# Performance work log

Measured on AMD Instinct MI355X. Metric: run time of the kernel, lower is better.

Reference implementation:

```python
import jax, jax.numpy as jnp
import numpy as np
from jax.scipy.special import gammaln

T_STEPS, N_GRID, NMUL = 730, 10000, 2
NEARZERO = 1e-5
LENF = 15  # unit-hydrograph length used by UH_gamma routing
STAT_NAMES = ["parFC", "parK0", "parK1", "parK2", "parLP", "parPERC", "parUZL",
              "parTT", "parCFMAX", "parCFR", "parCWH", "parC", "parRT", "parAC"]
BOUNDS = {"parBETA": (1.0, 6.0), "parFC": (50.0, 1000.0), "parK0": (0.05, 0.9),
          "parK1": (0.01, 0.5), "parK2": (0.001, 0.2), "parLP": (0.2, 1.0),
          "parPERC": (0.0, 10.0), "parUZL": (0.0, 100.0), "parTT": (-2.5, 2.5),
          "parCFMAX": (0.5, 10.0), "parCFR": (0.0, 0.1), "parCWH": (0.0, 0.2),
          "parBETAET": (0.3, 5.0), "parC": (0.0, 1.0), "parRT": (0.0, 20.0),
          "parAC": (0.0, 2500.0)}
ROUT_A = (0.0, 2.9)
ROUT_B = (0.0, 6.5)


def _scale(p, lo, hi):
    # change_param_range: affine map of [0,1]-normalized params to physical bounds
    return p * (hi - lo) + lo


def setup_inputs() -> dict:
    key = jax.random.key(0)
    ks = jax.random.split(key, 7)
    prcp = jax.random.uniform(ks[0], (T_STEPS, N_GRID)) * 10.0          # mm/day
    tmean = jax.random.uniform(ks[1], (T_STEPS, N_GRID)) * 30.0 - 10.0  # deg C, spans parTT range
    pet = jax.random.uniform(ks[2], (T_STEPS, N_GRID)) * 5.0            # mm/day
    x_phy = jnp.stack([prcp, tmean, pet], axis=-1).astype(jnp.float32)
    ac_all = jax.random.uniform(ks[3], (N_GRID,)) * 2500.0              # drainage area per unit basin
    elev_all = jax.random.uniform(ks[4], (N_GRID,)) * 3000.0            # elevation
    params_dy = jax.random.uniform(ks[5], (T_STEPS, N_GRID, 2 * NMUL))  # dynamic: parBETA, parBETAET
    params_stat = jax.random.uniform(ks[6], (N_GRID, 14 * NMUL + 2))    # 14 static phy + 2 routing
    return {"x_phy": x_phy, "ac_all": ac_all, "elev_all": elev_all,
            "params_dy": params_dy, "params_stat": params_stat}


def _forward(x_phy, ac_all, elev_all, params_dy, params_stat):
    T, G, _ = x_phy.shape
    P, Tair, PET = x_phy[..., 0], x_phy[..., 1], x_phy[..., 2]
    # expand forcing to nmul parameter components
    Pm = jnp.broadcast_to(P[..., None], (T, G, NMUL))
    Tm = jnp.broadcast_to(Tair[..., None], (T, G, NMUL))
    PETm = jnp.broadcast_to(PET[..., None], (T, G, NMUL))
    Ac = jnp.broadcast_to(ac_all[:, None], (G, NMUL))

    # dynamic (per-timestep) params; dy_drop=0.0 -> bernoulli drop mask is all zeros,
    # so the dynamic values are used directly at every step
    dy = params_dy.reshape(T, G, 2, NMUL)
    parBETA = _scale(dy[:, :, 0], *BOUNDS["parBETA"])
    parBETAET = _scale(dy[:, :, 1], *BOUNDS["parBETAET"])

    # static params: [G, 14, NMUL]
    stat = params_stat[:, :14 * NMUL].reshape(G, 14, NMUL)
    sp = {n: _scale(stat[:, i], *BOUNDS[n]) for i, n in enumerate(STAT_NAMES)}
    rout_a = _scale(params_stat[:, 14 * NMUL], *ROUT_A)
    rout_b = _scale(params_stat[:, 14 * NMUL + 1], *ROUT_B)

    def step(carry, xt):
        SNOWPACK, MELTWATER, SM, SUZ, SLZ = carry
        Pt, Tt, PETt, beta, betaet = xt
        rain_mask = (Tt >= sp["parTT"]).astype(Pt.dtype)
        RAIN = Pt * rain_mask
        SNOW = Pt * (1.0 - rain_mask)
        # --- snow bucket ---
        SNOWPACK = SNOWPACK + SNOW
        melt = jnp.maximum(sp["parCFMAX"] * (Tt - sp["parTT"]), 0.0)
        melt = jnp.minimum(melt, SNOWPACK)
        MELTWATER = MELTWATER + melt
        SNOWPACK = SNOWPACK - melt
        refreeze = jnp.maximum(sp["parCFR"] * sp["parCFMAX"] * (sp["parTT"] - Tt), 0.0)
        refreeze = jnp.minimum(refreeze, MELTWATER)
        SNOWPACK = SNOWPACK + refreeze
        MELTWATER = MELTWATER - refreeze
        tosoil = jnp.maximum(MELTWATER - sp["parCWH"] * SNOWPACK, 0.0)
        MELTWATER = MELTWATER - tosoil
        # --- soil bucket ---
        soil_wetness = jnp.clip((SM / sp["parFC"]) ** beta, 0.0, 1.0)
        recharge = (RAIN + tosoil) * soil_wetness
        SM = SM + RAIN + tosoil - recharge
        excess = jnp.maximum(SM - sp["parFC"], 0.0)
        SM = SM - excess
        evapfactor = jnp.clip(SM / (sp["parLP"] * sp["parFC"]), 0.0, 1.0) ** betaet
        ETact = jnp.minimum(SM, PETt * evapfactor)
        SM = jnp.maximum(SM - ETact, NEARZERO)
        # capillary rise from lower groundwater zone (parC)
        capillary = jnp.minimum(SLZ, sp["parC"] * SLZ * (1.0 - jnp.minimum(SM / sp["parFC"], 1.0)))
        SM = jnp.maximum(SM + capillary, NEARZERO)
        SLZ = jnp.maximum(SLZ - capillary, NEARZERO)
        # --- groundwater buckets ---
        SUZ = SUZ + recharge + excess
        PERC = jnp.minimum(SUZ, sp["parPERC"])
        SUZ = SUZ - PERC
        Q0 = sp["parK0"] * jnp.maximum(SUZ - sp["parUZL"], 0.0)
        SUZ = SUZ - Q0
        Q1 = sp["parK1"] * SUZ
        SUZ = SUZ - Q1
        SLZ = SLZ + PERC
        # HBV 2.0 regional groundwater loss (area-dependent via parRT / parAC; reconstructed)
        gw_loss = jnp.minimum(SLZ, sp["parRT"] * jnp.clip(1.0 - Ac / (sp["parAC"] + NEARZERO), 0.0, 1.0))
        SLZ = SLZ - gw_loss
        Q2 = sp["parK2"] * SLZ
        SLZ = SLZ - Q2
        Qt = Q0 + Q1 + Q2
        return (SNOWPACK, MELTWATER, SM, SUZ, SLZ), Qt

    init = tuple(jnp.full((G, NMUL), 1e-3, dtype=x_phy.dtype) for _ in range(5))
    _, Qsimmu = jax.lax.scan(step, init, (Pm, Tm, PETm, parBETA, parBETAET))
    Qsim = Qsimmu.mean(-1)  # [T, G]; muwts=None -> uniform average over nmul components

    # --- gamma unit-hydrograph routing (UH_gamma + causal UH_conv) ---
    a = jnp.maximum(rout_a, 0.0) + 0.1       # [G]
    theta = jnp.maximum(rout_b, 0.0) + 0.5   # [G]
    t = jnp.arange(LENF, dtype=Qsim.dtype) + 0.5  # [LENF]
    w = (jnp.exp(-gammaln(a))[None, :] * theta[None, :] ** (-a[None, :])
         * t[:, None] ** (a[None, :] - 1.0) * jnp.exp(-t[:, None] / theta[None, :]))
    w = w / w.sum(0)  # [LENF, G], normalized UH weights
    # causal grouped conv: flow[t] = sum_k w[k] * Qsim[t-k]
    Qpad = jnp.pad(Qsim, ((LENF - 1, 0), (0, 0)))
    flow = jnp.zeros_like(Qsim)
    for k in range(LENF):  # fixed, small tap count
        flow = flow + w[k][None, :] * Qpad[LENF - 1 - k: LENF - 1 - k + T]
    return flow[..., None]  # [T, G, 1] routed streamflow


def reference(x_phy, ac_all, elev_all, params_dy, params_stat):
    return _forward(x_phy, ac_all, elev_all, params_dy, params_stat)
```

## Files before the change

### kernel.cpp

```cpp
#include <hip/hip_runtime.h>


#define TS 730
#define NG 10000
#define CH 15
#define NCHUNK 49
#define XSTRIDE (NG * 3)
#define DSTRIDE (NG * 4)

#define AS1 __attribute__((address_space(1)))
#define AS3 __attribute__((address_space(3)))
#define WAIT_VMCNT(n) __builtin_amdgcn_s_waitcnt(((n) & 15) | 0x70 | 0xF00 | (((n) >> 4) << 14))
#define WAIT_LGKM0    __builtin_amdgcn_s_waitcnt(0xC07F)
#define SBAR          __builtin_amdgcn_s_barrier
#define SCHED_FENCE() __builtin_amdgcn_sched_barrier(0)

__device__ __forceinline__ void gload16(const float* g, float* l) {
    __builtin_amdgcn_global_load_lds((const AS1 void*)g, (AS3 void*)l, 16, 0, 0);
}
__device__ __forceinline__ float powpos(float x, float b) {
    return __builtin_amdgcn_exp2f(b * __builtin_amdgcn_logf(x));
}
__device__ __forceinline__ float med3(float x, float lo, float hi) {
    return __builtin_amdgcn_fmed3f(x, lo, hi);
}

__global__ __launch_bounds__(128, 1) void hbv_fused(
    const float* __restrict__ x_phy,
    const float* __restrict__ ac_all,
    const float* __restrict__ params_dy,
    const float* __restrict__ params_stat,
    float* __restrict__ out)
{
    __shared__ float xls0[1536], xls1[1536];
    __shared__ float dls0[2048], dls1[2048];
    __shared__ float qb0[960], qb1[960];

    const int tid  = threadIdx.x;
    const int wid  = tid >> 6;
    const int lane = tid & 63;
    const int m    = lane >> 5;
    const int cell = lane & 31;
    const int g0   = blockIdx.x * 32;
    const int g    = g0 + cell;
    const int gl   = g < NG ? g : NG - 1;
    const int g0r  = (g0 <= NG - 32) ? g0 : NG - 32;
    const int co   = cell + (g0 - g0r);
    const int cl   = co < 31 ? co : 31;

    const float* ps = params_stat + (size_t)gl * 30;
    const float FC    = ps[0  + m] * 950.f   + 50.f;
    const float K0    = ps[2  + m] * 0.85f   + 0.05f;
    const float K1    = ps[4  + m] * 0.49f   + 0.01f;
    const float K2    = ps[6  + m] * 0.199f  + 0.001f;
    const float LP    = ps[8  + m] * 0.8f    + 0.2f;
    const float PERCp = ps[10 + m] * 10.f;
    const float UZL   = ps[12 + m] * 100.f;
    const float TTp   = ps[14 + m] * 5.f     - 2.5f;
    const float CFMAX = ps[16 + m] * 9.5f    + 0.5f;
    const float CFR   = ps[18 + m] * 0.1f;
    const float CWH   = ps[20 + m] * 0.2f;
    const float Cc    = ps[22 + m];
    const float RT    = ps[24 + m] * 20.f;
    const float ACp   = ps[26 + m] * 2500.f;
    const float ra    = ps[28] * 2.9f;
    const float rb    = ps[29] * 6.5f;

    const float Acv     = ac_all[gl];
    const float invFC   = 1.f / FC;
    const float invLPFC = 1.f / (LP * FC);
    const float nCFRC   = -(CFR * CFMAX);
    const float gwcap   = RT * fminf(fmaxf(1.f - Acv / (ACp + 1e-5f), 0.f), 1.f);

    const float a     = fmaxf(ra, 0.f) + 0.1f;
    const float th    = fmaxf(rb, 0.f) + 0.5f;
    const float am1   = a - 1.f;
    const float nl2e  = 1.44269504f / th;
    float w[CH];
    float wsum = 0.f;
#pragma unroll
    for (int k = 0; k < CH; ++k) {
        const float tk = (float)k + 0.5f;
        const float v  = __builtin_amdgcn_exp2f(am1 * __builtin_amdgcn_logf(tk) - tk * nl2e);
        w[k] = v; wsum += v;
    }
    const float wn = 0.5f / wsum;
#pragma unroll
    for (int k = 0; k < CH; ++k) w[k] *= wn;

    int offx[6], offd[8];
#pragma unroll
    for (int i = 0; i < 6; ++i) {
        int idx = i * 64 + lane;
        idx = idx < 360 ? idx : 359;
        const int row = idx / 24;
        const int col = idx - row * 24;
        offx[i] = row * XSTRIDE + col * 4;
    }
#pragma unroll
    for (int i = 0; i < 8; ++i) {
        int idx = i * 64 + lane;
        idx = idx < 480 ? idx : 479;
        const int row = idx >> 5;
        const int col = idx & 31;
        offd[i] = row * DSTRIDE + col * 4;
    }
    const float* xbase = x_phy     + (size_t)g0r * 3;
    const float* dbase = params_dy + (size_t)g0r * 4;

    auto issue = [&](int cc, float* xl, float* dl) {
        if (cc == NCHUNK - 1) {
#pragma unroll
            for (int i = 0; i < 6; ++i) {
                int idx = i * 64 + lane; idx = idx < 360 ? idx : 359;
                const int row = idx / 24, col = idx - row * 24;
                int t = cc * CH + row; t = t < TS ? t : TS - 1;
                gload16(xbase + (size_t)t * XSTRIDE + col * 4, xl + i * 256);
            }
#pragma unroll
            for (int i = 0; i < 8; ++i) {
                int idx = i * 64 + lane; idx = idx < 480 ? idx : 479;
                const int row = idx >> 5, col = idx & 31;
                int t = cc * CH + row; t = t < TS ? t : TS - 1;
                gload16(dbase + (size_t)t * DSTRIDE + col * 4, dl + i * 256);
            }
        } else {
            const float* xp = xbase + (size_t)cc * CH * XSTRIDE;
            const float* dp = dbase + (size_t)cc * CH * DSTRIDE;
#pragma unroll
            for (int i = 0; i < 6; ++i) gload16(xp + offx[i], xl + i * 256);
#pragma unroll
            for (int i = 0; i < 8; ++i) gload16(dp + offd[i], dl + i * 256);
        }
    };

    if (wid == 0) {
        float SP = 1e-3f, MW = 1e-3f, SM = 1e-3f, SUZ = 1e-3f, SLZ = 1e-3f;
        float CcSLZ = Cc * 1e-3f;

        auto scan = [&](const float* xl, const float* dl, float* qb) {
            float Pc = xl[cl * 3 + 0], Tc = xl[cl * 3 + 1], Ec = xl[cl * 3 + 2];
            float4 dvc = *(const float4*)&dl[cl * 4];
#pragma unroll
            for (int j = 0; j < CH; ++j) {
                float Pn, Tn, En; float4 dvn;
                if (j < CH - 1) {
                    Pn  = xl[(j + 1) * 96 + cl * 3 + 0];
                    Tn  = xl[(j + 1) * 96 + cl * 3 + 1];
                    En  = xl[(j + 1) * 96 + cl * 3 + 2];
                    dvn = *(const float4*)&dl[(j + 1) * 128 + cl * 4];
                }
                const float beta   = fmaf(m ? dvc.y : dvc.x, 5.f, 1.f);
                const float betaet = fmaf(m ? dvc.w : dvc.z, 4.7f, 0.3f);

                const float t1   = Tc - TTp;
                const float snow = (t1 < 0.f) ? Pc : 0.f;
                const float rain = Pc - snow;
                SP += snow;
                const float melt = med3(CFMAX * t1, 0.f, SP);
                MW += melt; SP -= melt;
                const float refr = med3(nCFRC * t1, 0.f, MW);
                SP += refr; MW -= refr;
                const float tosoil = fmaxf(MW - CWH * SP, 0.f);
                MW -= tosoil;

                const float sw  = fminf(powpos(SM * invFC, beta), 1.f);
                const float rts = rain + tosoil;
                SM = fmaf(rts, 1.f - sw, SM);
                const float exc = fmaxf(SM - FC, 0.f);
                SM = fminf(SM, FC);
                const float ef = powpos(fminf(SM * invLPFC, 1.f), betaet);
                SM = fmaxf(SM - Ec * ef, 1e-5f);
                const float cap = CcSLZ * fmaxf(1.f - SM * invFC, 0.f);
                SM  = fmaxf(SM + cap, 1e-5f);
                SLZ = fmaxf(SLZ - cap, 1e-5f);

                SUZ = SUZ + rts * sw + exc;
                const float perc = fminf(SUZ, PERCp);
                SUZ -= perc;
                const float Q0 = K0 * fmaxf(SUZ - UZL, 0.f);
                SUZ -= Q0;
                const float Q1 = K1 * SUZ;
                SUZ -= Q1;
                SLZ += perc;
                SLZ = fmaxf(SLZ - gwcap, 0.f);
                const float Q2 = K2 * SLZ;
                SLZ -= Q2;
                CcSLZ = Cc * SLZ;
                qb[(j << 6) + lane] = Q0 + Q1 + Q2;

                Pc = Pn; Tc = Tn; Ec = En; dvc = dvn;
            }
        };

        SBAR();
        scan(xls0, dls0, qb0);
        WAIT_LGKM0; SCHED_FENCE();
        for (int cp = 0; cp < 24; ++cp) {
            SBAR();
            scan(xls1, dls1, qb1);
            WAIT_LGKM0; SCHED_FENCE();
            SBAR();
            scan(xls0, dls0, qb0);
            WAIT_LGKM0; SCHED_FENCE();
        }
        SBAR();
    } else {
        float facc[CH];
#pragma unroll
        for (int k = 0; k < CH; ++k) facc[k] = 0.f;
        const bool doStore = (g < NG) && (lane < 32);
        const int  l32 = lane & 31;

        auto conv = [&](int c, const float* qb) {
            float* op = out + (size_t)c * CH * NG + g;
            const int tb = c * CH;
#pragma unroll
            for (int j = 0; j < CH; ++j) {
                const float qm = qb[(j << 6) + l32] + qb[(j << 6) + 32 + l32];
#pragma unroll
                for (int k = 0; k < CH; ++k)
                    facc[(j + k) % CH] = fmaf(w[k], qm, facc[(j + k) % CH]);
                if (doStore && (tb + j < TS)) op[(size_t)j * NG] = facc[j];
                facc[j] = 0.f;
            }
        };

        issue(0, xls0, dls0);
        WAIT_VMCNT(0); SCHED_FENCE();
        SBAR();
        issue(1, xls1, dls1);
        WAIT_VMCNT(0); SCHED_FENCE();
        SBAR();
        for (int cp = 0; cp < 24; ++cp) {
            issue(2 * cp + 2, xls0, dls0);
            conv(2 * cp, qb0);
            WAIT_VMCNT(15); SCHED_FENCE();
            SBAR();
            if (cp < 23) issue(2 * cp + 3, xls1, dls1);
            conv(2 * cp + 1, qb1);
            WAIT_VMCNT(15); SCHED_FENCE();
            SBAR();
        }
        conv(48, qb0);
    }
}

extern "C" void kernel_launch(void* const* d_in, const int* in_sizes, int n_in,
                              void* d_out, int out_size, void* d_ws, size_t ws_size,
                              hipStream_t stream) {
    const float* x_phy = (const float*)d_in[0];
    const float* ac    = (const float*)d_in[1];
    const float* pdy   = (const float*)d_in[3];
    const float* pst   = (const float*)d_in[4];
    float* out = (float*)d_out;

    const int grid = (NG + 31) / 32;
    hbv_fused<<<grid, 128, 0, stream>>>(x_phy, ac, pdy, pst, out);
}
```

Before: 276.0 us.

## Split scan into snow and soil wavefronts pipelined with loader/conv wave

```diff
diff --git a/kernel.cpp b/kernel.cpp
--- a/kernel.cpp
+++ b/kernel.cpp
@@ -25,15 +25,16 @@
     return __builtin_amdgcn_fmed3f(x, lo, hi);
 }
 
-__global__ __launch_bounds__(128, 1) void hbv_fused(
+__global__ __launch_bounds__(192, 1) void hbv_fused(
     const float* __restrict__ x_phy,
     const float* __restrict__ ac_all,
     const float* __restrict__ params_dy,
     const float* __restrict__ params_stat,
     float* __restrict__ out)
 {
-    __shared__ float xls0[1536], xls1[1536];
-    __shared__ float dls0[2048], dls1[2048];
+    __shared__ float xls0[1536], xls1[1536], xls2[1536], xls3[1536];
+    __shared__ float dls0[2048], dls1[2048], dls2[2048], dls3[2048];
+    __shared__ float rb0[960], rb1[960];
     __shared__ float qb0[960], qb1[960];
 
     const int tid  = threadIdx.x;
@@ -63,8 +64,6 @@
     const float Cc    = ps[22 + m];
     const float RT    = ps[24 + m] * 20.f;
     const float ACp   = ps[26 + m] * 2500.f;
-    const float ra    = ps[28] * 2.9f;
-    const float rb    = ps[29] * 6.5f;
 
     const float Acv     = ac_all[gl];
     const float invFC   = 1.f / FC;
@@ -72,87 +71,17 @@
     const float nCFRC   = -(CFR * CFMAX);
     const float gwcap   = RT * fminf(fmaxf(1.f - Acv / (ACp + 1e-5f), 0.f), 1.f);
 
-    const float a     = fmaxf(ra, 0.f) + 0.1f;
-    const float th    = fmaxf(rb, 0.f) + 0.5f;
-    const float am1   = a - 1.f;
-    const float nl2e  = 1.44269504f / th;
-    float w[CH];
-    float wsum = 0.f;
-#pragma unroll
-    for (int k = 0; k < CH; ++k) {
-        const float tk = (float)k + 0.5f;
-        const float v  = __builtin_amdgcn_exp2f(am1 * __builtin_amdgcn_logf(tk) - tk * nl2e);
-        w[k] = v; wsum += v;
-    }
-    const float wn = 0.5f / wsum;
-#pragma unroll
-    for (int k = 0; k < CH; ++k) w[k] *= wn;
-
-    int offx[6], offd[8];
-#pragma unroll
-    for (int i = 0; i < 6; ++i) {
-        int idx = i * 64 + lane;
-        idx = idx < 360 ? idx : 359;
-        const int row = idx / 24;
-        const int col = idx - row * 24;
-        offx[i] = row * XSTRIDE + col * 4;
-    }
-#pragma unroll
-    for (int i = 0; i < 8; ++i) {
-        int idx = i * 64 + lane;
-        idx = idx < 480 ? idx : 479;
-        const int row = idx >> 5;
-        const int col = idx & 31;
-        offd[i] = row * DSTRIDE + col * 4;
-    }
-    const float* xbase = x_phy     + (size_t)g0r * 3;
-    const float* dbase = params_dy + (size_t)g0r * 4;
-
-    auto issue = [&](int cc, float* xl, float* dl) {
-        if (cc == NCHUNK - 1) {
-#pragma unroll
-            for (int i = 0; i < 6; ++i) {
-                int idx = i * 64 + lane; idx = idx < 360 ? idx : 359;
-                const int row = idx / 24, col = idx - row * 24;
-                int t = cc * CH + row; t = t < TS ? t : TS - 1;
-                gload16(xbase + (size_t)t * XSTRIDE + col * 4, xl + i * 256);
-            }
-#pragma unroll
-            for (int i = 0; i < 8; ++i) {
-                int idx = i * 64 + lane; idx = idx < 480 ? idx : 479;
-                const int row = idx >> 5, col = idx & 31;
-                int t = cc * CH + row; t = t < TS ? t : TS - 1;
-                gload16(dbase + (size_t)t * DSTRIDE + col * 4, dl + i * 256);
-            }
-        } else {
-            const float* xp = xbase + (size_t)cc * CH * XSTRIDE;
-            const float* dp = dbase + (size_t)cc * CH * DSTRIDE;
-#pragma unroll
-            for (int i = 0; i < 6; ++i) gload16(xp + offx[i], xl + i * 256);
-#pragma unroll
-            for (int i = 0; i < 8; ++i) gload16(dp + offd[i], dl + i * 256);
-        }
-    };
-
     if (wid == 0) {
-        float SP = 1e-3f, MW = 1e-3f, SM = 1e-3f, SUZ = 1e-3f, SLZ = 1e-3f;
-        float CcSLZ = Cc * 1e-3f;
-
-        auto scan = [&](const float* xl, const float* dl, float* qb) {
-            float Pc = xl[cl * 3 + 0], Tc = xl[cl * 3 + 1], Ec = xl[cl * 3 + 2];
-            float4 dvc = *(const float4*)&dl[cl * 4];
+        float SP = 1e-3f, MW = 1e-3f;
+        auto snowc = [&](const float* xl, float* rbuf) {
+            float Pc = xl[cl * 3 + 0], Tc = xl[cl * 3 + 1];
 #pragma unroll
             for (int j = 0; j < CH; ++j) {
-                float Pn, Tn, En; float4 dvn;
+                float Pn, Tn;
                 if (j < CH - 1) {
-                    Pn  = xl[(j + 1) * 96 + cl * 3 + 0];
-                    Tn  = xl[(j + 1) * 96 + cl * 3 + 1];
-                    En  = xl[(j + 1) * 96 + cl * 3 + 2];
-                    dvn = *(const float4*)&dl[(j + 1) * 128 + cl * 4];
-                }
-                const float beta   = fmaf(m ? dvc.y : dvc.x, 5.f, 1.f);
-                const float betaet = fmaf(m ? dvc.w : dvc.z, 4.7f, 0.3f);
-
+                    Pn = xl[(j + 1) * 96 + cl * 3 + 0];
+                    Tn = xl[(j + 1) * 96 + cl * 3 + 1];
+                }
                 const float t1   = Tc - TTp;
                 const float snow = (t1 < 0.f) ? Pc : 0.f;
                 const float rain = Pc - snow;
@@ -163,9 +92,40 @@
                 SP += refr; MW -= refr;
                 const float tosoil = fmaxf(MW - CWH * SP, 0.f);
                 MW -= tosoil;
+                rbuf[(j << 6) + lane] = rain + tosoil;
+                Pc = Pn; Tc = Tn;
+            }
+        };
+        SBAR();
+        for (int cq = 0; cq < 12; ++cq) {
+            snowc(xls0, rb0); WAIT_LGKM0; SCHED_FENCE(); SBAR();
+            snowc(xls1, rb1); WAIT_LGKM0; SCHED_FENCE(); SBAR();
+            snowc(xls2, rb0); WAIT_LGKM0; SCHED_FENCE(); SBAR();
+            snowc(xls3, rb1); WAIT_LGKM0; SCHED_FENCE(); SBAR();
+        }
+        snowc(xls0, rb0); WAIT_LGKM0; SCHED_FENCE(); SBAR();
+        SBAR();
+    } else if (wid == 1) {
+        float SM = 1e-3f, SUZ = 1e-3f, SLZ = 1e-3f;
+        float CcSLZ = Cc * 1e-3f;
+        auto soilc = [&](const float* xl, const float* dl,
+                         const float* rbuf, float* qbuf) {
+            float Ec   = xl[cl * 3 + 2];
+            float4 dvc = *(const float4*)&dl[cl * 4];
+            float rtsc = rbuf[lane];
+#pragma unroll
+            for (int j = 0; j < CH; ++j) {
+                float En, rtsn; float4 dvn;
+                if (j < CH - 1) {
+                    En   = xl[(j + 1) * 96 + cl * 3 + 2];
+                    dvn  = *(const float4*)&dl[(j + 1) * 128 + cl * 4];
+                    rtsn = rbuf[((j + 1) << 6) + lane];
+                }
+                const float beta   = fmaf(m ? dvc.y : dvc.x, 5.f, 1.f);
+                const float betaet = fmaf(m ? dvc.w : dvc.z, 4.7f, 0.3f);
 
                 const float sw  = fminf(powpos(SM * invFC, beta), 1.f);
-                const float rts = rain + tosoil;
+                const float rts = rtsc;
                 SM = fmaf(rts, 1.f - sw, SM);
                 const float exc = fmaxf(SM - FC, 0.f);
                 SM = fminf(SM, FC);
@@ -187,30 +147,90 @@
                 const float Q2 = K2 * SLZ;
                 SLZ -= Q2;
                 CcSLZ = Cc * SLZ;
-                qb[(j << 6) + lane] = Q0 + Q1 + Q2;
-
-                Pc = Pn; Tc = Tn; Ec = En; dvc = dvn;
-            }
-        };
-
-        SBAR();
-        scan(xls0, dls0, qb0);
-        WAIT_LGKM0; SCHED_FENCE();
-        for (int cp = 0; cp < 24; ++cp) {
-            SBAR();
-            scan(xls1, dls1, qb1);
-            WAIT_LGKM0; SCHED_FENCE();
-            SBAR();
-            scan(xls0, dls0, qb0);
-            WAIT_LGKM0; SCHED_FENCE();
-        }
-        SBAR();
+                qbuf[(j << 6) + lane] = Q0 + Q1 + Q2;
+
+                Ec = En; dvc = dvn; rtsc = rtsn;
+            }
+        };
+        SBAR();
+        SBAR();
+        for (int cq = 0; cq < 12; ++cq) {
+            soilc(xls0, dls0, rb0, qb0); WAIT_LGKM0; SCHED_FENCE(); SBAR();
+            soilc(xls1, dls1, rb1, qb1); WAIT_LGKM0; SCHED_FENCE(); SBAR();
+            soilc(xls2, dls2, rb0, qb0); WAIT_LGKM0; SCHED_FENCE(); SBAR();
+            soilc(xls3, dls3, rb1, qb1); WAIT_LGKM0; SCHED_FENCE(); SBAR();
+        }
+        soilc(xls0, dls0, rb0, qb0); WAIT_LGKM0; SCHED_FENCE(); SBAR();
     } else {
+        const float ra = ps[28] * 2.9f;
+        const float rb = ps[29] * 6.5f;
+        const float a    = fmaxf(ra, 0.f) + 0.1f;
+        const float th   = fmaxf(rb, 0.f) + 0.5f;
+        const float am1  = a - 1.f;
+        const float nl2e = 1.44269504f / th;
+        float w[CH];
+        float wsum = 0.f;
+#pragma unroll
+        for (int k = 0; k < CH; ++k) {
+            const float tk = (float)k + 0.5f;
+            const float v  = __builtin_amdgcn_exp2f(am1 * __builtin_amdgcn_logf(tk) - tk * nl2e);
+            w[k] = v; wsum += v;
+        }
+        const float wn = 0.5f / wsum;
+#pragma unroll
+        for (int k = 0; k < CH; ++k) w[k] *= wn;
+
+        int offx[6], offd[8];
+#pragma unroll
+        for (int i = 0; i < 6; ++i) {
+            int idx = i * 64 + lane;
+            idx = idx < 360 ? idx : 359;
+            const int row = idx / 24;
+            const int col = idx - row * 24;
+            offx[i] = row * XSTRIDE + col * 4;
+        }
+#pragma unroll
+        for (int i = 0; i < 8; ++i) {
+            int idx = i * 64 + lane;
+            idx = idx < 480 ? idx : 479;
+            const int row = idx >> 5;
+            const int col = idx & 31;
+            offd[i] = row * DSTRIDE + col * 4;
+        }
+        const float* xbase = x_phy     + (size_t)g0r * 3;
+        const float* dbase = params_dy + (size_t)g0r * 4;
+
+        auto issue = [&](int cc, float* xl, float* dl) {
+            if (cc == NCHUNK - 1) {
+#pragma unroll
+                for (int i = 0; i < 6; ++i) {
+                    int idx = i * 64 + lane; idx = idx < 360 ? idx : 359;
+                    const int row = idx / 24, col = idx - row * 24;
+                    int t = cc * CH + row; t = t < TS ? t : TS - 1;
+                    gload16(xbase + (size_t)t * XSTRIDE + col * 4, xl + i * 256);
+                }
+#pragma unroll
+                for (int i = 0; i < 8; ++i) {
+                    int idx = i * 64 + lane; idx = idx < 480 ? idx : 479;
+                    const int row = idx >> 5, col = idx & 31;
+                    int t = cc * CH + row; t = t < TS ? t : TS - 1;
+                    gload16(dbase + (size_t)t * DSTRIDE + col * 4, dl + i * 256);
+                }
+            } else {
+                const float* xp = xbase + (size_t)cc * CH * XSTRIDE;
+                const float* dp = dbase + (size_t)cc * CH * DSTRIDE;
+#pragma unroll
+                for (int i = 0; i < 6; ++i) gload16(xp + offx[i], xl + i * 256);
+#pragma unroll
+                for (int i = 0; i < 8; ++i) gload16(dp + offd[i], dl + i * 256);
+            }
+        };
+
         float facc[CH];
 #pragma unroll
         for (int k = 0; k < CH; ++k) facc[k] = 0.f;
-        const bool doStore = (g < NG) && (lane < 32);
-        const int  l32 = lane & 31;
+        const bool doStore = (g < NG);
+        const int  l32 = cell;
 
         auto conv = [&](int c, const float* qb) {
             float* op = out + (size_t)c * CH * NG + g;
@@ -221,27 +241,36 @@
 #pragma unroll
                 for (int k = 0; k < CH; ++k)
                     facc[(j + k) % CH] = fmaf(w[k], qm, facc[(j + k) % CH]);
-                if (doStore && (tb + j < TS)) op[(size_t)j * NG] = facc[j];
+                if (doStore && (lane < 32) && (tb + j < TS))
+                    op[(size_t)j * NG] = facc[j];
                 facc[j] = 0.f;
             }
         };
 
         issue(0, xls0, dls0);
-        WAIT_VMCNT(0); SCHED_FENCE();
-        SBAR();
         issue(1, xls1, dls1);
-        WAIT_VMCNT(0); SCHED_FENCE();
-        SBAR();
-        for (int cp = 0; cp < 24; ++cp) {
-            issue(2 * cp + 2, xls0, dls0);
-            conv(2 * cp, qb0);
-            WAIT_VMCNT(15); SCHED_FENCE();
-            SBAR();
-            if (cp < 23) issue(2 * cp + 3, xls1, dls1);
-            conv(2 * cp + 1, qb1);
-            WAIT_VMCNT(15); SCHED_FENCE();
-            SBAR();
-        }
+        WAIT_VMCNT(14); SCHED_FENCE(); SBAR();
+        issue(2, xls2, dls2);
+        WAIT_VMCNT(14); SCHED_FENCE(); SBAR();
+        issue(3, xls3, dls3);
+        WAIT_VMCNT(14); SCHED_FENCE(); SBAR();
+        issue(4, xls0, dls0); conv(0, qb0);
+        WAIT_VMCNT(29); SCHED_FENCE(); SBAR();
+        for (int np = 0; np < 11; ++np) {
+            const int n = 3 + 4 * np;
+            issue(n + 2, xls1, dls1); conv(n - 2, qb1);
+            WAIT_VMCNT(44); SCHED_FENCE(); SBAR();
+            issue(n + 3, xls2, dls2); conv(n - 1, qb0);
+            WAIT_VMCNT(44); SCHED_FENCE(); SBAR();
+            issue(n + 4, xls3, dls3); conv(n,     qb1);
+            WAIT_VMCNT(44); SCHED_FENCE(); SBAR();
+            issue(n + 5, xls0, dls0); conv(n + 1, qb0);
+            WAIT_VMCNT(44); SCHED_FENCE(); SBAR();
+        }
+        conv(45, qb1);
+        WAIT_VMCNT(30); SCHED_FENCE(); SBAR();
+        conv(46, qb0); SBAR();
+        conv(47, qb1); SBAR();
         conv(48, qb0);
     }
 }
@@ -256,5 +285,5 @@
     float* out = (float*)d_out;
 
     const int grid = (NG + 31) / 32;
-    hbv_fused<<<grid, 128, 0, stream>>>(x_phy, ac, pdy, pst, out);
-}
+    hbv_fused<<<grid, 192, 0, stream>>>(x_phy, ac, pdy, pst, out);
+}
```

After: 258.7 us. 6.3% less time.
